# Kernel tuning notes

Measured on AMD Instinct MI355X. Metric: run time of the kernel, lower is better.

## Reference

```python
import jax, jax.numpy as jnp
import numpy as np
from jax import lax

EPS = 1e-5

def layer_norm(x, w, b):
    mu = x.mean(-1, keepdims=True)
    var = ((x - mu) ** 2).mean(-1, keepdims=True)
    return (x - mu) * lax.rsqrt(var + EPS) * w + b

def causal_dw_conv(x, w, b):
    # x: [B,L,D], w: [D,K] depthwise kernel, causal left pad
    B, L, D = x.shape
    K = w.shape[1]
    xt = jnp.pad(x.transpose(0, 2, 1), ((0, 0), (0, 0), (K - 1, 0)))  # [B,D,L+K-1]
    y = lax.conv_general_dilated(xt, w[:, None, :], (1,), 'VALID',
                                 dimension_numbers=('NCH', 'OIH', 'NCH'),
                                 feature_group_count=D)
    return (y + b[:, None]).transpose(0, 2, 1)

def mamba_block(x, ln_w, ln_b, W_in, b_in, conv_w, conv_b, W_xproj, W_dt, b_dt, A_log, Dp, W_out, b_out):
    res = x
    x = layer_norm(x, ln_w, ln_b)
    xz = x @ W_in + b_in                      # [B,L,2*Di]
    Di = xz.shape[-1] // 2
    xp, z = xz[..., :Di], xz[..., Di:]
    xp = jax.nn.silu(causal_dw_conv(xp, conv_w, conv_b))
    dbl = xp @ W_xproj                        # [B,L,R+2N]
    N = A_log.shape[-1]
    R = dbl.shape[-1] - 2 * N
    dt, Bm, Cm = dbl[..., :R], dbl[..., R:R + N], dbl[..., R + N:]
    delta = jax.nn.softplus(dt @ W_dt + b_dt)  # [B,L,Di]
    A = -jnp.exp(A_log)                        # [Di,N]
    dA = jnp.exp(delta[..., None] * A)                         # [B,L,Di,N]
    dBx = delta[..., None] * Bm[:, :, None, :] * xp[..., None]  # [B,L,Di,N]

    def step(h, inp):
        dAt, dBxt, ct = inp
        h = dAt * h + dBxt
        return h, jnp.einsum('bdn,bn->bd', h, ct)

    h0 = jnp.zeros((x.shape[0], Di, N), x.dtype)
    _, ys = lax.scan(step, h0, (dA.transpose(1, 0, 2, 3), dBx.transpose(1, 0, 2, 3), Cm.transpose(1, 0, 2)))
    y = ys.transpose(1, 0, 2) + xp * Dp        # [B,L,Di]
    y = y * jax.nn.silu(z)
    return res + y @ W_out + b_out

def reference(x, ln_w, ln_b, W_in, b_in, conv_w, conv_b, W_xproj, W_dt, b_dt, A_log, D, W_out, b_out, Wg, bg, Wv, bv):
    fwd = mamba_block(x, ln_w[0], ln_b[0], W_in[0], b_in[0], conv_w[0], conv_b[0], W_xproj[0], W_dt[0], b_dt[0], A_log[0], D[0], W_out[0], b_out[0])
    bwd = mamba_block(x[:, ::-1], ln_w[1], ln_b[1], W_in[1], b_in[1], conv_w[1], conv_b[1], W_xproj[1], W_dt[1], b_dt[1], A_log[1], D[1], W_out[1], b_out[1])
    bwd = bwd[:, ::-1]
    comb = jnp.concatenate([fwd, bwd], -1)
    gate = jax.nn.sigmoid(comb @ Wg + bg)
    value = comb @ Wv + bv
    return (gate * value + (1.0 - gate) * fwd + (1.0 - gate) * bwd) / 2.0

def setup_inputs() -> dict:
    B, L, Dm = 2, 1024, 1024
    Di, N, R, K = 2048, 16, 64, 4
    key = jax.random.key(0)
    ks = jax.random.split(key, 12)
    s_in = 1.0 / np.sqrt(Dm)
    s_di = 1.0 / np.sqrt(Di)
    A = jnp.broadcast_to(jnp.arange(1, N + 1, dtype=jnp.float32), (Di, N))
    return {
        'x': jax.random.normal(ks[0], (B, L, Dm), jnp.float32),
        'ln_w': jnp.ones((2, Dm), jnp.float32),
        'ln_b': jnp.zeros((2, Dm), jnp.float32),
        'W_in': jax.random.normal(ks[1], (2, Dm, 2 * Di), jnp.float32) * s_in,
        'b_in': jnp.zeros((2, 2 * Di), jnp.float32),
        'conv_w': jax.random.normal(ks[2], (2, Di, K), jnp.float32) * 0.5,
        'conv_b': jnp.zeros((2, Di), jnp.float32),
        'W_xproj': jax.random.normal(ks[3], (2, Di, R + 2 * N), jnp.float32) * s_di,
        'W_dt': jax.random.normal(ks[4], (2, R, Di), jnp.float32) * 0.02,
        'b_dt': jnp.full((2, Di), -4.6, jnp.float32) + 0.1 * jax.random.normal(ks[5], (2, Di), jnp.float32),
        'A_log': jnp.log(jnp.stack([A, A])),
        'D': jnp.ones((2, Di), jnp.float32),
        'W_out': jax.random.normal(ks[6], (2, Di, Dm), jnp.float32) * s_di,
        'b_out': jnp.zeros((2, Dm), jnp.float32),
        'Wg': jax.random.normal(ks[7], (2 * Dm, Dm), jnp.float32) / np.sqrt(2 * Dm),
        'bg': jnp.zeros((Dm,), jnp.float32),
        'Wv': jax.random.normal(ks[8], (2 * Dm, Dm), jnp.float32) / np.sqrt(2 * Dm),
        'bv': jnp.zeros((Dm,), jnp.float32),
    }
```

## Files before the change

### kernel.cpp

```cpp
#include <hip/hip_runtime.h>
#include <math.h>

constexpr int BB = 2;
constexpr int LL = 1024;
constexpr int DM = 1024;
constexpr int DI = 2048;
constexpr int NS = 16;
constexpr int RR = 64;
constexpr int MROWS = BB * LL;

constexpr int CLEN = 32;
constexpr int NCH = LL / CLEN;

constexpr int LDT = 40;
constexpr int NSPLIT = 16;
constexpr int KCH = DI / NSPLIT;

#define DEV __device__ __forceinline__

typedef unsigned short ushort_t;
using bf16x8 = __attribute__((ext_vector_type(8))) short;
using f32x4  = __attribute__((ext_vector_type(4))) float;

DEV float sigmoidf_(float x) { return 1.f / (1.f + expf(-x)); }
DEV float siluf_(float x) { return x * sigmoidf_(x); }
DEV float fast_softplus(float x) {
    return fmaxf(x, 0.f) + __logf(1.f + __expf(-fabsf(x)));
}

DEV ushort_t f2bf(float x) {
    union { float f; unsigned u; } v; v.f = x;
    unsigned r = v.u + 0x7FFFu + ((v.u >> 16) & 1u);
    return (ushort_t)(r >> 16);
}
DEV float bf2f(ushort_t u) {
    union { unsigned u; float f; } v; v.u = ((unsigned)u) << 16;
    return v.f;
}

typedef const __attribute__((address_space(1))) unsigned int* gptr_t;
typedef __attribute__((address_space(3))) unsigned int* lptr_t;
DEV void gload16(const void* g, void* l) {
    __builtin_amdgcn_global_load_lds((gptr_t)g, (lptr_t)l, 16, 0, 0);
}

template <int N> DEV void waitvm();
template <> DEV void waitvm<0>() { asm volatile("s_waitcnt vmcnt(0)" ::: "memory"); }
template <> DEV void waitvm<6>() { asm volatile("s_waitcnt vmcnt(6)" ::: "memory"); }
template <> DEV void waitvm<8>() { asm volatile("s_waitcnt vmcnt(8)" ::: "memory"); }
DEV void barrier_() { __builtin_amdgcn_s_barrier(); }

__global__ __launch_bounds__(256) void tcast(
    const float* __restrict__ in, long sIn,
    ushort_t* __restrict__ outT, long sOut,
    int R, int C)
{
    in += (size_t)blockIdx.z * sIn;
    outT += (size_t)blockIdx.z * sOut;
    __shared__ float tile[64][65];
    int r0 = blockIdx.y * 64, c0 = blockIdx.x * 64;
#pragma unroll
    for (int i = 0; i < 4; ++i) {
        int r = (threadIdx.x >> 4) + i * 16;
        int c4 = (threadIdx.x & 15) * 4;
        float4 v = *reinterpret_cast<const float4*>(&in[(size_t)(r0 + r) * C + c0 + c4]);
        tile[r][c4] = v.x; tile[r][c4 + 1] = v.y; tile[r][c4 + 2] = v.z; tile[r][c4 + 3] = v.w;
    }
    __syncthreads();
#pragma unroll
    for (int i = 0; i < 2; ++i) {
        int c = (threadIdx.x >> 3) + i * 32;
        int r8 = (threadIdx.x & 7) * 8;
        ushort_t o[8];
#pragma unroll
        for (int j = 0; j < 8; ++j) o[j] = f2bf(tile[r8 + j][c]);
        *reinterpret_cast<int4*>(&outT[(size_t)(c0 + c) * R + r0 + r8]) =
            *reinterpret_cast<int4*>(o);
    }
}

__global__ __launch_bounds__(256) void tcastP(
    const float* __restrict__ in, long sIn,
    ushort_t* __restrict__ outT, long sOut,
    int R, int C)
{
    in += (size_t)blockIdx.z * sIn;
    outT += (size_t)blockIdx.z * sOut;
    int idx = blockIdx.x * 256 + threadIdx.x;
    if (idx >= R * C) return;
    int r = idx / C, c = idx - r * C;
    outT[(size_t)c * R + r] = f2bf(in[idx]);
}

__global__ __launch_bounds__(256) void ln_kernel(
    const float* __restrict__ x,
    const float* __restrict__ ln_w,
    const float* __restrict__ ln_b,
    ushort_t* __restrict__ xlnb)
{
    int row = blockIdx.x;
    const float* xr = x + (size_t)row * DM;
    int i4 = threadIdx.x * 4;
    float4 v = *reinterpret_cast<const float4*>(&xr[i4]);
    float s = v.x + v.y + v.z + v.w;
    float s2 = v.x * v.x + v.y * v.y + v.z * v.z + v.w * v.w;
    for (int off = 32; off > 0; off >>= 1) {
        s += __shfl_down(s, off);
        s2 += __shfl_down(s2, off);
    }
    __shared__ float sbuf[10];
    int wid = threadIdx.x >> 6;
    if ((threadIdx.x & 63) == 0) { sbuf[wid] = s; sbuf[4 + wid] = s2; }
    __syncthreads();
    if (threadIdx.x == 0) {
        float S = sbuf[0] + sbuf[1] + sbuf[2] + sbuf[3];
        float S2 = sbuf[4] + sbuf[5] + sbuf[6] + sbuf[7];
        float mu = S / DM;
        float var = S2 / DM - mu * mu;
        sbuf[8] = mu;
        sbuf[9] = rsqrtf(var + 1e-5f);
    }
    __syncthreads();
    float mu = sbuf[8], rstd = sbuf[9];
    float nv0 = (v.x - mu) * rstd, nv1 = (v.y - mu) * rstd;
    float nv2 = (v.z - mu) * rstd, nv3 = (v.w - mu) * rstd;
#pragma unroll
    for (int d = 0; d < 2; ++d) {
        float4 w = *reinterpret_cast<const float4*>(&ln_w[d * DM + i4]);
        float4 b = *reinterpret_cast<const float4*>(&ln_b[d * DM + i4]);
        ushort_t o[4];
        o[0] = f2bf(nv0 * w.x + b.x);
        o[1] = f2bf(nv1 * w.y + b.y);
        o[2] = f2bf(nv2 * w.z + b.z);
        o[3] = f2bf(nv3 * w.w + b.w);
        *reinterpret_cast<uint2*>(&xlnb[(size_t)d * MROWS * DM + (size_t)row * DM + i4]) =
            *reinterpret_cast<uint2*>(o);
    }
}

__global__ __launch_bounds__(512, 1) void gemm_xpz256(
    const ushort_t* __restrict__ A,
    const ushort_t* __restrict__ Bt,
    const float* __restrict__ bias,
    ushort_t* __restrict__ xpb,
    ushort_t* __restrict__ zb)
{
    __shared__ ushort_t lds[4 * 256 * 64];

    int bid = blockIdx.x;
    int sid = (bid & 7) * 32 + (bid >> 3);
    int z = sid >> 7;
    int rem = sid & 127;
    int bx = rem >> 3;
    int by = rem & 7;
    int row0 = by * 256, col0 = bx * 256;

    A += (size_t)z * MROWS * DM;
    Bt += (size_t)z * (2 * DI) * DM;
    bias += (size_t)z * (2 * DI);
    xpb += (size_t)z * MROWS * DI;
    zb += (size_t)z * MROWS * DI;

    int tid = threadIdx.x;
    int lane = tid & 63;
    int w = tid >> 6;
    int wr = w >> 2, wc = w & 3;
    int lrow = lane & 15, lk = lane >> 4;
    int cr = lane >> 3, cs = lane & 7;

    f32x4 acc[8][4];
#pragma unroll
    for (int m = 0; m < 8; ++m)
#pragma unroll
        for (int n = 0; n < 4; ++n) acc[m][n] = {0.f, 0.f, 0.f, 0.f};

    auto stage = [&](int buf, int k0) {
        ushort_t* As_ = lds + buf * (256 * 64);
        ushort_t* Bs_ = lds + (2 + buf) * (256 * 64);
#pragma unroll
        for (int j = 0; j < 8; ++j) {
            int c = j * 8 + w;
            if (c < 32) {
                int r = c * 8 + cr;
                gload16(&A[(size_t)(row0 + r) * DM + k0 + ((cs ^ (r & 7)) * 8)],
                        As_ + c * 512);
            } else {
                int r = (c - 32) * 8 + cr;
                gload16(&Bt[(size_t)(col0 + r) * DM + k0 + ((cs ^ (r & 7)) * 8)],
                        Bs_ + (c - 32) * 512);
            }
        }
    };
    auto compute = [&](int buf) {
        const ushort_t* As_ = lds + buf * (256 * 64);
        const ushort_t* Bs_ = lds + (2 + buf) * (256 * 64);
#pragma unroll
        for (int kk = 0; kk < 2; ++kk) {
            int lkk = kk * 4 + lk;
            bf16x8 af[8], bfr[4];
#pragma unroll
            for (int m = 0; m < 8; ++m) {
                int ar = wr * 128 + m * 16 + lrow;
                af[m] = *reinterpret_cast<const bf16x8*>(&As_[ar * 64 + ((lkk ^ (ar & 7)) * 8)]);
            }
#pragma unroll
            for (int n = 0; n < 4; ++n) {
                int br = wc * 64 + n * 16 + lrow;
                bfr[n] = *reinterpret_cast<const bf16x8*>(&Bs_[br * 64 + ((lkk ^ (br & 7)) * 8)]);
            }
#pragma unroll
            for (int m = 0; m < 8; ++m)
#pragma unroll
                for (int n = 0; n < 4; ++n)
                    acc[m][n] = __builtin_amdgcn_mfma_f32_16x16x32_bf16(af[m], bfr[n], acc[m][n], 0, 0, 0);
        }
    };

    stage(0, 0);
    stage(1, 64);
    waitvm<8>();
    barrier_();
    for (int t = 0; t < 16; ++t) {
        int buf = t & 1;
        compute(buf);
        barrier_();
        int kn = (t + 2) * 64;
        if (kn < 1024) {
            stage(buf, kn);
            waitvm<8>();
        } else {
            waitvm<0>();
        }
        barrier_();
    }

    constexpr int EP2 = 264;
    ushort_t* dst = (col0 < DI) ? (xpb + col0) : (zb + (col0 - DI));
    __syncthreads();
#pragma unroll
    for (int h = 0; h < 2; ++h) {
        if (wr == h) {
#pragma unroll
            for (int n = 0; n < 4; ++n) {
                int col = wc * 64 + n * 16 + lrow;
                float bv = bias[col0 + col];
#pragma unroll
                for (int m = 0; m < 8; ++m)
#pragma unroll
                    for (int rr = 0; rr < 4; ++rr) {
                        int rl = m * 16 + lk * 4 + rr;
                        lds[rl * EP2 + col] = f2bf(acc[m][n][rr] + bv);
                    }
            }
        }
        __syncthreads();
#pragma unroll
        for (int q = 0; q < 8; ++q) {
            int lin = q * 512 + tid;
            int r = lin >> 5, c8 = lin & 31;
            *reinterpret_cast<int4*>(&dst[(size_t)(row0 + h * 128 + r) * DI + c8 * 8]) =
                *reinterpret_cast<int4*>(&lds[r * EP2 + c8 * 8]);
        }
        __syncthreads();
    }
}

enum { EPI_XPZ = 0, EPI_COMB = 1, EPI_SOFT = 2 };

template <int BM, int EPI>
__global__ __launch_bounds__(256) void gemm_as(
    const ushort_t* __restrict__ A, int lda, long sA,
    const ushort_t* __restrict__ Bt, int ldb, long sB,
    const float* __restrict__ bias, long sBias,
    ushort_t* __restrict__ outB, long sOutB,
    ushort_t* __restrict__ outB2, long sOutB2,
    const float* __restrict__ res,
    int ldout, int Kdim)
{
    constexpr int FM = BM / 32;
    constexpr int CA = BM / 8;
    constexpr int CT = CA + 16;
    constexpr int LW = CT / 4;
    __shared__ ushort_t lds[2 * BM * 64 + 2 * 128 * 64];

    int z = blockIdx.z;
    A += (size_t)z * sA; Bt += (size_t)z * sB; bias += (size_t)z * sBias;
    outB += (size_t)z * sOutB;
    if (outB2) outB2 += (size_t)z * sOutB2;

    int tid = threadIdx.x;
    int lane = tid & 63;
    int w = tid >> 6, wr = w >> 1, wc = w & 1;
    int lrow = lane & 15, lk = lane >> 4;
    int cr = lane >> 3, cs = lane & 7;
    int row0 = blockIdx.y * BM, col0 = blockIdx.x * 128;

    f32x4 acc[FM][4];
#pragma unroll
    for (int m = 0; m < FM; ++m)
#pragma unroll
        for (int n = 0; n < 4; ++n) acc[m][n] = {0.f, 0.f, 0.f, 0.f};

    auto stage = [&](int buf, int k0) {
        ushort_t* As_ = lds + buf * (BM * 64);
        ushort_t* Bs_ = lds + 2 * BM * 64 + buf * (128 * 64);
#pragma unroll
        for (int j = 0; j < CT / 4; ++j) {
            int c = j * 4 + w;
            if (c < CA) {
                int r = c * 8 + cr;
                gload16(&A[(size_t)(row0 + r) * lda + k0 + ((cs ^ (r & 7)) * 8)],
                        As_ + c * 512);
            } else {
                int r = (c - CA) * 8 + cr;
                gload16(&Bt[(size_t)(col0 + r) * ldb + k0 + ((cs ^ (r & 7)) * 8)],
                        Bs_ + (c - CA) * 512);
            }
        }
    };
    auto compute = [&](int buf) {
        const ushort_t* As_ = lds + buf * (BM * 64);
        const ushort_t* Bs_ = lds + 2 * BM * 64 + buf * (128 * 64);
#pragma unroll
        for (int kk = 0; kk < 2; ++kk) {
            int lkk = kk * 4 + lk;
            bf16x8 af[FM], bfr[4];
#pragma unroll
            for (int m = 0; m < FM; ++m) {
                int ar = wr * (BM / 2) + m * 16 + lrow;
                af[m] = *reinterpret_cast<const bf16x8*>(&As_[ar * 64 + ((lkk ^ (ar & 7)) * 8)]);
            }
#pragma unroll
            for (int n = 0; n < 4; ++n) {
                int br = wc * 64 + n * 16 + lrow;
                bfr[n] = *reinterpret_cast<const bf16x8*>(&Bs_[br * 64 + ((lkk ^ (br & 7)) * 8)]);
            }
#pragma unroll
            for (int m = 0; m < FM; ++m)
#pragma unroll
                for (int n = 0; n < 4; ++n)
                    acc[m][n] = __builtin_amdgcn_mfma_f32_16x16x32_bf16(af[m], bfr[n], acc[m][n], 0, 0, 0);
        }
    };

    stage(0, 0);
    if (Kdim > 64) {
        stage(1, 64);
        waitvm<LW>();
    } else {
        waitvm<0>();
    }
    barrier_();
    int nt = Kdim >> 6;
    for (int t = 0; t < nt; ++t) {
        int buf = t & 1;
        compute(buf);
        barrier_();
        int kn = (t + 2) * 64;
        if (kn < Kdim) {
            stage(buf, kn);
            waitvm<LW>();
        } else {
            waitvm<0>();
        }
        barrier_();
    }

    constexpr int EP = 136;
    __syncthreads();
#pragma unroll
    for (int n = 0; n < 4; ++n) {
        int col = wc * 64 + n * 16 + lrow;
        float bv = bias[col0 + col];
#pragma unroll
        for (int m = 0; m < FM; ++m) {
#pragma unroll
            for (int rr = 0; rr < 4; ++rr) {
                int rl = wr * (BM / 2) + m * 16 + lk * 4 + rr;
                float v = acc[m][n][rr] + bv;
                if constexpr (EPI == EPI_COMB)
                    v += res[(size_t)(row0 + rl) * DM + col0 + col];
                else if constexpr (EPI == EPI_SOFT)
                    v = fast_softplus(v);
                lds[rl * EP + col] = f2bf(v);
            }
        }
    }
    __syncthreads();
    const ushort_t* dst;
    if constexpr (EPI == EPI_XPZ) dst = (col0 < DI) ? outB + col0 : outB2 + (col0 - DI);
    else dst = outB + col0;
    constexpr int NI = BM * 16 / 256;
#pragma unroll
    for (int q = 0; q < NI; ++q) {
        int lin = q * 256 + tid;
        int r = lin >> 4, c8 = lin & 15;
        *reinterpret_cast<int4*>(const_cast<ushort_t*>(&dst[(size_t)(row0 + r) * ldout + c8 * 8])) =
            *reinterpret_cast<int4*>(&lds[r * EP + c8 * 8]);
    }
}

__global__ __launch_bounds__(256) void gemm_final64(
    const ushort_t* __restrict__ combb,
    const ushort_t* __restrict__ Bg,
    const ushort_t* __restrict__ Bv,
    const float* __restrict__ bgp, const float* __restrict__ bvp,
    float* __restrict__ out)
{
    __shared__ ushort_t lds[6 * 64 * 64];

    int tid = threadIdx.x;
    int lane = tid & 63;
    int w = tid >> 6, wr = w >> 1, wc = w & 1;
    int lrow = lane & 15, lk = lane >> 4;
    int cr = lane >> 3, cs = lane & 7;
    int row0 = blockIdx.y * 64, col0 = blockIdx.x * 64;

    f32x4 accg[2][2], accv[2][2];
#pragma unroll
    for (int m = 0; m < 2; ++m)
#pragma unroll
        for (int n = 0; n < 2; ++n) { accg[m][n] = {0.f,0.f,0.f,0.f}; accv[m][n] = {0.f,0.f,0.f,0.f}; }

    auto stage = [&](int buf, int k0) {
        ushort_t* As_  = lds + buf * 4096;
        ushort_t* Bs1_ = lds + 8192 + buf * 4096;
        ushort_t* Bs2_ = lds + 16384 + buf * 4096;
#pragma unroll
        for (int j = 0; j < 6; ++j) {
            int c = j * 4 + w;
            if (c < 8) {
                int r = c * 8 + cr;
                gload16(&combb[(size_t)(row0 + r) * (2 * DM) + k0 + ((cs ^ (r & 7)) * 8)],
                        As_ + c * 512);
            } else if (c < 16) {
                int r = (c - 8) * 8 + cr;
                gload16(&Bg[(size_t)(col0 + r) * (2 * DM) + k0 + ((cs ^ (r & 7)) * 8)],
                        Bs1_ + (c - 8) * 512);
            } else {
                int r = (c - 16) * 8 + cr;
                gload16(&Bv[(size_t)(col0 + r) * (2 * DM) + k0 + ((cs ^ (r & 7)) * 8)],
                        Bs2_ + (c - 16) * 512);
            }
        }
    };
    auto compute = [&](int buf) {
        const ushort_t* As_  = lds + buf * 4096;
        const ushort_t* Bs1_ = lds + 8192 + buf * 4096;
        const ushort_t* Bs2_ = lds + 16384 + buf * 4096;
#pragma unroll
        for (int kk = 0; kk < 2; ++kk) {
            int lkk = kk * 4 + lk;
            bf16x8 af[2], b1[2], b2[2];
#pragma unroll
            for (int m = 0; m < 2; ++m) {
                int ar = wr * 32 + m * 16 + lrow;
                af[m] = *reinterpret_cast<const bf16x8*>(&As_[ar * 64 + ((lkk ^ (ar & 7)) * 8)]);
            }
#pragma unroll
            for (int n = 0; n < 2; ++n) {
                int br = wc * 32 + n * 16 + lrow;
                b1[n] = *reinterpret_cast<const bf16x8*>(&Bs1_[br * 64 + ((lkk ^ (br & 7)) * 8)]);
                b2[n] = *reinterpret_cast<const bf16x8*>(&Bs2_[br * 64 + ((lkk ^ (br & 7)) * 8)]);
            }
#pragma unroll
            for (int m = 0; m < 2; ++m)
#pragma unroll
                for (int n = 0; n < 2; ++n) {
                    accg[m][n] = __builtin_amdgcn_mfma_f32_16x16x32_bf16(af[m], b1[n], accg[m][n], 0, 0, 0);
                    accv[m][n] = __builtin_amdgcn_mfma_f32_16x16x32_bf16(af[m], b2[n], accv[m][n], 0, 0, 0);
                }
        }
    };

    stage(0, 0);
    stage(1, 64);
    waitvm<6>();
    barrier_();
    for (int t = 0; t < 32; ++t) {
        int buf = t & 1;
        compute(buf);
        barrier_();
        int kn = (t + 2) * 64;
        if (kn < 2 * DM) {
            stage(buf, kn);
            waitvm<6>();
        } else {
            waitvm<0>();
        }
        barrier_();
    }

    constexpr int EPF = 68;
    float* epf = (float*)lds;
    __syncthreads();
#pragma unroll
    for (int n = 0; n < 2; ++n) {
        int col = wc * 32 + n * 16 + lrow;
        float bgv = bgp[col0 + col];
        float bvv = bvp[col0 + col];
#pragma unroll
        for (int m = 0; m < 2; ++m) {
#pragma unroll
            for (int rr = 0; rr < 4; ++rr) {
                int rl = wr * 32 + m * 16 + lk * 4 + rr;
                float g = sigmoidf_(accg[m][n][rr] + bgv);
                float v = accv[m][n][rr] + bvv;
                float f = bf2f(combb[(size_t)(row0 + rl) * (2 * DM) + col0 + col]);
                float wv2 = bf2f(combb[(size_t)(row0 + rl) * (2 * DM) + DM + col0 + col]);
                epf[rl * EPF + col] = 0.5f * (g * v + (1.f - g) * (f + wv2));
            }
        }
    }
    __syncthreads();
#pragma unroll
    for (int q = 0; q < 4; ++q) {
        int lin = q * 256 + tid;
        int r = lin >> 4, c4 = lin & 15;
        *reinterpret_cast<float4*>(&out[(size_t)(row0 + r) * DM + col0 + c4 * 4]) =
            *reinterpret_cast<float4*>(&epf[r * EPF + c4 * 4]);
    }
}

__global__ __launch_bounds__(256) void gemm_xproj(
    const ushort_t* __restrict__ A,
    const ushort_t* __restrict__ Bt,
    float* __restrict__ part)
{
    int z = blockIdx.z;
    A += (size_t)z * MROWS * DI;
    Bt += (size_t)z * 96 * DI;
    part += (size_t)z * NSPLIT * MROWS * 96;

    __shared__ ushort_t As[128 * LDT];
    __shared__ ushort_t Bs[96 * LDT];
    int tid = threadIdx.x;
    int lane = tid & 63;
    int w = tid >> 6, wr = w >> 1, wc = w & 1;
    int lrow = lane & 15, lk = lane >> 4;
    int s = blockIdx.x, rt = blockIdx.y;
    int row0 = rt * 128;
    int k0 = s * KCH;

    f32x4 acc[4][3];
#pragma unroll
    for (int m = 0; m < 4; ++m)
#pragma unroll
        for (int n = 0; n < 3; ++n) acc[m][n] = {0.f, 0.f, 0.f, 0.f};

    int sr = tid >> 2, ss = tid & 3;
    const ushort_t* ga0 = A + (size_t)(row0 + sr) * DI + k0 + ss * 8;
    const ushort_t* ga1 = A + (size_t)(row0 + sr + 64) * DI + k0 + ss * 8;

    for (int kk = 0; kk < KCH; kk += 32) {
        int4 a0 = *reinterpret_cast<const int4*>(ga0);
        int4 a1 = *reinterpret_cast<const int4*>(ga1);
        ga0 += 32; ga1 += 32;
        __syncthreads();
        *reinterpret_cast<int4*>(&As[sr * LDT + ss * 8]) = a0;
        *reinterpret_cast<int4*>(&As[(sr + 64) * LDT + ss * 8]) = a1;
        for (int i = tid; i < 96 * 4; i += 256) {
            int br = i >> 2, bs = i & 3;
            *reinterpret_cast<int4*>(&Bs[br * LDT + bs * 8]) =
                *reinterpret_cast<const int4*>(&Bt[(size_t)br * DI + k0 + kk + bs * 8]);
        }
        __syncthreads();
        bf16x8 af[4], bfr[3];
#pragma unroll
        for (int m = 0; m < 4; ++m)
            af[m] = *reinterpret_cast<const bf16x8*>(&As[(wr * 64 + m * 16 + lrow) * LDT + lk * 8]);
#pragma unroll
        for (int n = 0; n < 3; ++n)
            bfr[n] = *reinterpret_cast<const bf16x8*>(&Bs[(wc * 48 + n * 16 + lrow) * LDT + lk * 8]);
#pragma unroll
        for (int m = 0; m < 4; ++m)
#pragma unroll
            for (int n = 0; n < 3; ++n)
                acc[m][n] = __builtin_amdgcn_mfma_f32_16x16x32_bf16(af[m], bfr[n], acc[m][n], 0, 0, 0);
    }

#pragma unroll
    for (int n = 0; n < 3; ++n) {
        int col = wc * 48 + n * 16 + lrow;
#pragma unroll
        for (int m = 0; m < 4; ++m) {
#pragma unroll
            for (int rr = 0; rr < 4; ++rr) {
                int row = row0 + wr * 64 + m * 16 + lk * 4 + rr;
                part[((size_t)s * MROWS + row) * 96 + col] = acc[m][n][rr];
            }
        }
    }
}

__global__ __launch_bounds__(256) void dbl_reduce(
    const float* __restrict__ part,
    float* __restrict__ dblf,
    ushort_t* __restrict__ dtb)
{
    int idx = blockIdx.x * 256 + threadIdx.x;
    int d = idx / (MROWS * 96);
    int rem = idx - d * (MROWS * 96);
    int row = rem / 96, col = rem - row * 96;
    const float* p = part + (size_t)d * NSPLIT * MROWS * 96;
    float v = 0.f;
#pragma unroll
    for (int s = 0; s < NSPLIT; ++s)
        v += p[((size_t)s * MROWS + row) * 96 + col];
    dblf[idx] = v;
    if (col < RR) dtb[(size_t)d * MROWS * RR + (size_t)row * RR + col] = f2bf(v);
}

__global__ __launch_bounds__(256) void conv_silu_kernel(
    const ushort_t* __restrict__ xpb,
    const float* __restrict__ cw,
    const float* __restrict__ cb,
    ushort_t* __restrict__ xpcb)
{
    int d = blockIdx.y;
    xpb += (size_t)d * MROWS * DI;
    cw += (size_t)d * DI * 4;
    cb += (size_t)d * DI;
    xpcb += (size_t)d * MROWS * DI;
    int idx = blockIdx.x * 256 + threadIdx.x;
    int c = idx & (DI - 1);
    int row = idx >> 11;
    int t = row & (LL - 1);
    int b = row >> 10;
    float w0 = cw[c * 4 + 0], w1 = cw[c * 4 + 1], w2 = cw[c * 4 + 2], w3 = cw[c * 4 + 3];
    float acc = cb[c];
    if (!d) {
#pragma unroll
        for (int k = 0; k < 4; ++k) {
            int tt = t - 3 + k;
            if (tt >= 0) {
                float wv = (k == 0) ? w0 : (k == 1) ? w1 : (k == 2) ? w2 : w3;
                acc = fmaf(wv, bf2f(xpb[(size_t)(b * LL + tt) * DI + c]), acc);
            }
        }
    } else {
#pragma unroll
        for (int k = 0; k < 4; ++k) {
            int tt = t + 3 - k;
            if (tt < LL) {
                float wv = (k == 0) ? w0 : (k == 1) ? w1 : (k == 2) ? w2 : w3;
                acc = fmaf(wv, bf2f(xpb[(size_t)(b * LL + tt) * DI + c]), acc);
            }
        }
    }
    xpcb[idx] = f2bf(siluf_(acc));
}

__global__ __launch_bounds__(256) void scan_part1(
    const ushort_t* __restrict__ deltab,
    const ushort_t* __restrict__ xpcb,
    const float* __restrict__ dblf,
    const float* __restrict__ A_log,
    float* __restrict__ chunkS,
    ushort_t* __restrict__ chunkH)
{
    int zz = blockIdx.z;
    int d = zz >> 1, b = zz & 1;
    const ushort_t* delta_d = deltab + (size_t)d * MROWS * DI;
    const ushort_t* xpc_d = xpcb + (size_t)d * MROWS * DI;
    const float* dbl_d = dblf + (size_t)d * MROWS * 96;
    const float* Alg = A_log + (size_t)d * DI * NS;
    int reverse = d;

    int c = blockIdx.x * 256 + threadIdx.x;
    int ch = blockIdx.y;
    int base = b * LL;

    __shared__ float sB[CLEN][16];
    for (int r = threadIdx.x >> 4; r < CLEN; r += 16) {
        int col = threadIdx.x & 15;
        int i = ch * CLEN + r;
        int t = reverse ? (LL - 1 - i) : i;
        sB[r][col] = dbl_d[(size_t)(base + t) * 96 + RR + col];
    }
    __syncthreads();

    float Ac[NS];
#pragma unroll
    for (int q = 0; q < 4; ++q) {
        float4 a = *reinterpret_cast<const float4*>(&Alg[(size_t)c * NS + q * 4]);
        Ac[q * 4 + 0] = -__expf(a.x);
        Ac[q * 4 + 1] = -__expf(a.y);
        Ac[q * 4 + 2] = -__expf(a.z);
        Ac[q * 4 + 3] = -__expf(a.w);
    }
    float h[NS] = {};
    float S = 0.f;
    for (int ii = 0; ii < CLEN; ++ii) {
        int i = ch * CLEN + ii;
        int t = reverse ? (LL - 1 - i) : i;
        size_t row = (size_t)(base + t);
        float dlt = bf2f(delta_d[row * DI + c]);
        float xv = bf2f(xpc_d[row * DI + c]);
        S += dlt;
        float dx = dlt * xv;
        float4 B0 = *reinterpret_cast<const float4*>(&sB[ii][0]);
        float4 B1 = *reinterpret_cast<const float4*>(&sB[ii][4]);
        float4 B2 = *reinterpret_cast<const float4*>(&sB[ii][8]);
        float4 B3 = *reinterpret_cast<const float4*>(&sB[ii][12]);
        float Bv[NS] = {B0.x, B0.y, B0.z, B0.w, B1.x, B1.y, B1.z, B1.w,
                        B2.x, B2.y, B2.z, B2.w, B3.x, B3.y, B3.z, B3.w};
#pragma unroll
        for (int n = 0; n < NS; ++n)
            h[n] = fmaf(__expf(dlt * Ac[n]), h[n], dx * Bv[n]);
    }
    size_t sidx = ((size_t)((d * BB + b) * NCH + ch)) * DI + c;
    chunkS[sidx] = S;
    ushort_t o[16];
#pragma unroll
    for (int n = 0; n < NS; ++n) o[n] = f2bf(h[n]);
    ushort_t* hp = chunkH + sidx * NS;
    *reinterpret_cast<int4*>(&hp[0]) = *reinterpret_cast<int4*>(&o[0]);
    *reinterpret_cast<int4*>(&hp[8]) = *reinterpret_cast<int4*>(&o[8]);
}

__global__ __launch_bounds__(256) void scan_part2(
    ushort_t* __restrict__ chunkH,
    const float* __restrict__ chunkS,
    const float* __restrict__ A_log)
{
    int idx = blockIdx.x * 256 + threadIdx.x;
    int d = idx >> 16;
    int r = idx & 65535;
    int n = r & 15;
    int c = (r >> 4) & (DI - 1);
    int b = r >> 15;
    float Ac = -__expf(A_log[(size_t)d * DI * NS + (size_t)c * NS + n]);
    float cur = 0.f;
    for (int j = 0; j < NCH; ++j) {
        size_t sidx = ((size_t)((d * BB + b) * NCH + j)) * DI + c;
        float S = chunkS[sidx];
        float hf = bf2f(chunkH[sidx * NS + n]);
        float nxt = fmaf(__expf(Ac * S), cur, hf);
        chunkH[sidx * NS + n] = f2bf(cur);
        cur = nxt;
    }
}

__global__ __launch_bounds__(256) void scan_part3(
    const ushort_t* __restrict__ deltab,
    const ushort_t* __restrict__ xpcb,
    const float* __restrict__ dblf,
    const ushort_t* __restrict__ zbuf,
    const float* __restrict__ A_log,
    const float* __restrict__ Dp,
    const ushort_t* __restrict__ chunkH,
    ushort_t* __restrict__ ybufb)
{
    int zz = blockIdx.z;
    int d = zz >> 1, b = zz & 1;
    const ushort_t* delta_d = deltab + (size_t)d * MROWS * DI;
    const ushort_t* xpc_d = xpcb + (size_t)d * MROWS * DI;
    const float* dbl_d = dblf + (size_t)d * MROWS * 96;
    const ushort_t* z_d = zbuf + (size_t)d * MROWS * DI;
    const float* Alg = A_log + (size_t)d * DI * NS;
    const float* Dp_d = Dp + (size_t)d * DI;
    ushort_t* y_d = ybufb + (size_t)d * MROWS * DI;
    int reverse = d;

    int c = blockIdx.x * 256 + threadIdx.x;
    int ch = blockIdx.y;
    int base = b * LL;

    __shared__ float sBC[CLEN][32];
    for (int r = threadIdx.x >> 5; r < CLEN; r += 8) {
        int col = threadIdx.x & 31;
        int i = ch * CLEN + r;
        int t = reverse ? (LL - 1 - i) : i;
        sBC[r][col] = dbl_d[(size_t)(base + t) * 96 + RR + col];
    }
    __syncthreads();

    float Ac[NS];
#pragma unroll
    for (int q = 0; q < 4; ++q) {
        float4 a = *reinterpret_cast<const float4*>(&Alg[(size_t)c * NS + q * 4]);
        Ac[q * 4 + 0] = -__expf(a.x);
        Ac[q * 4 + 1] = -__expf(a.y);
        Ac[q * 4 + 2] = -__expf(a.z);
        Ac[q * 4 + 3] = -__expf(a.w);
    }
    size_t sidx = ((size_t)((d * BB + b) * NCH + ch)) * DI + c;
    const ushort_t* hp = chunkH + sidx * NS;
    int4 h0 = *reinterpret_cast<const int4*>(&hp[0]);
    int4 h1 = *reinterpret_cast<const int4*>(&hp[8]);
    const ushort_t* hs0 = reinterpret_cast<const ushort_t*>(&h0);
    const ushort_t* hs1 = reinterpret_cast<const ushort_t*>(&h1);
    float h[NS];
#pragma unroll
    for (int n = 0; n < 8; ++n) { h[n] = bf2f(hs0[n]); h[8 + n] = bf2f(hs1[n]); }
    float Dc = Dp_d[c];
    for (int ii = 0; ii < CLEN; ++ii) {
        int i = ch * CLEN + ii;
        int t = reverse ? (LL - 1 - i) : i;
        size_t row = (size_t)(base + t);
        float dlt = bf2f(delta_d[row * DI + c]);
        float xv = bf2f(xpc_d[row * DI + c]);
        float dx = dlt * xv;
        float4 B0 = *reinterpret_cast<const float4*>(&sBC[ii][0]);
        float4 B1 = *reinterpret_cast<const float4*>(&sBC[ii][4]);
        float4 B2 = *reinterpret_cast<const float4*>(&sBC[ii][8]);
        float4 B3 = *reinterpret_cast<const float4*>(&sBC[ii][12]);
        float4 C0 = *reinterpret_cast<const float4*>(&sBC[ii][16]);
        float4 C1 = *reinterpret_cast<const float4*>(&sBC[ii][20]);
        float4 C2 = *reinterpret_cast<const float4*>(&sBC[ii][24]);
        float4 C3 = *reinterpret_cast<const float4*>(&sBC[ii][28]);
        float Bv[NS] = {B0.x, B0.y, B0.z, B0.w, B1.x, B1.y, B1.z, B1.w,
                        B2.x, B2.y, B2.z, B2.w, B3.x, B3.y, B3.z, B3.w};
        float Cv[NS] = {C0.x, C0.y, C0.z, C0.w, C1.x, C1.y, C1.z, C1.w,
                        C2.x, C2.y, C2.z, C2.w, C3.x, C3.y, C3.z, C3.w};
        float y = 0.f;
#pragma unroll
        for (int n = 0; n < NS; ++n) {
            h[n] = fmaf(__expf(dlt * Ac[n]), h[n], dx * Bv[n]);
            y = fmaf(h[n], Cv[n], y);
        }
        float z = bf2f(z_d[row * DI + c]);
        y_d[row * DI + c] = f2bf((y + xv * Dc) * siluf_(z));
    }
}

extern "C" void kernel_launch(void* const* d_in, const int* in_sizes, int n_in,
                              void* d_out, int out_size, void* d_ws, size_t ws_size,
                              hipStream_t stream)
{
    const float* x      = (const float*)d_in[0];
    const float* ln_w   = (const float*)d_in[1];
    const float* ln_b   = (const float*)d_in[2];
    const float* W_in   = (const float*)d_in[3];
    const float* b_in   = (const float*)d_in[4];
    const float* conv_w = (const float*)d_in[5];
    const float* conv_b = (const float*)d_in[6];
    const float* W_xproj= (const float*)d_in[7];
    const float* W_dt   = (const float*)d_in[8];
    const float* b_dt   = (const float*)d_in[9];
    const float* A_log  = (const float*)d_in[10];
    const float* Dp     = (const float*)d_in[11];
    const float* W_out  = (const float*)d_in[12];
    const float* b_out  = (const float*)d_in[13];
    const float* Wg     = (const float*)d_in[14];
    const float* bg     = (const float*)d_in[15];
    const float* Wv     = (const float*)d_in[16];
    const float* bv     = (const float*)d_in[17];
    float* out = (float*)d_out;

    ushort_t* sb = (ushort_t*)d_ws;
    size_t o = 0;
    ushort_t* R0 = sb + o;
    ushort_t* xlnb = R0;
    ushort_t* xpb  = R0 + (size_t)2 * MROWS * DM;
    o += (size_t)2 * MROWS * DM + (size_t)2 * MROWS * DI;
    float* part = (float*)R0;
    ushort_t* ybufb = R0;
    ushort_t* zb     = sb + o; o += (size_t)2 * MROWS * DI;
    ushort_t* xpcb   = sb + o; o += (size_t)2 * MROWS * DI;
    ushort_t* deltab = sb + o; o += (size_t)2 * MROWS * DI;
    ushort_t* chHb   = sb + o; o += (size_t)2 * BB * NCH * DI * NS;
    ushort_t* combb  = sb + o; o += (size_t)MROWS * 2 * DM;
    float* dblf = (float*)combb;
    ushort_t* dtb = combb + (size_t)2 * (2 * MROWS * 96);
    float* chS = (float*)(combb + (size_t)2 * (2 * MROWS * 96) + (size_t)2 * MROWS * RR);
    ushort_t* WTin   = sb + o; o += (size_t)2 * (2 * DI) * DM;
    ushort_t* WTout  = sb + o; o += (size_t)2 * DM * DI;
    ushort_t* WTgv   = sb + o; o += (size_t)2 * DM * (2 * DM);
    ushort_t* WTxp   = sb + o; o += (size_t)2 * 96 * DI;
    ushort_t* WTdt   = sb + o; o += (size_t)2 * DI * RR;

    tcast<<<dim3(DM / 64, DI / 64, 2), 256, 0, stream>>>(
        W_out, (long)DI * DM, WTout, (long)DM * DI, DI, DM);
    tcast<<<dim3(DM / 64, (2 * DM) / 64, 1), 256, 0, stream>>>(
        Wg, 0, WTgv, 0, 2 * DM, DM);
    tcast<<<dim3(DM / 64, (2 * DM) / 64, 1), 256, 0, stream>>>(
        Wv, 0, WTgv + (size_t)DM * 2 * DM, 0, 2 * DM, DM);
    tcast<<<dim3(DI / 64, RR / 64, 2), 256, 0, stream>>>(
        W_dt, (long)RR * DI, WTdt, (long)DI * RR, RR, DI);
    tcastP<<<dim3((DI * 96 + 255) / 256, 1, 2), 256, 0, stream>>>(
        W_xproj, (long)DI * 96, WTxp, (long)96 * DI, DI, 96);
    tcast<<<dim3((2 * DI) / 64, DM / 64, 2), 256, 0, stream>>>(
        W_in, (long)DM * 2 * DI, WTin, (long)(2 * DI) * DM, DM, 2 * DI);

    ln_kernel<<<MROWS, 256, 0, stream>>>(x, ln_w, ln_b, xlnb);

    gemm_xpz256<<<256, 512, 0, stream>>>(xlnb, WTin, b_in, xpb, zb);

    conv_silu_kernel<<<dim3((MROWS * DI) / 256, 2), 256, 0, stream>>>(
        xpb, conv_w, conv_b, xpcb);

    gemm_xproj<<<dim3(NSPLIT, MROWS / 128, 2), 256, 0, stream>>>(xpcb, WTxp, part);
    dbl_reduce<<<(2 * MROWS * 96) / 256, 256, 0, stream>>>(part, dblf, dtb);

    gemm_as<128, EPI_SOFT><<<dim3(DI / 128, MROWS / 128, 2), 256, 0, stream>>>(
        dtb, RR, (long)MROWS * RR, WTdt, RR, (long)DI * RR,
        b_dt, DI, deltab, (long)MROWS * DI, nullptr, 0, nullptr, DI, RR);

    scan_part1<<<dim3(DI / 256, NCH, 4), 256, 0, stream>>>(
        deltab, xpcb, dblf, A_log, chS, chHb);
    scan_part2<<<(2 * BB * DI * NS) / 256, 256, 0, stream>>>(chHb, chS, A_log);
    scan_part3<<<dim3(DI / 256, NCH, 4), 256, 0, stream>>>(
        deltab, xpcb, dblf, zb, A_log, Dp, chHb, ybufb);

    gemm_as<64, EPI_COMB><<<dim3(DM / 128, MROWS / 64, 2), 256, 0, stream>>>(
        ybufb, DI, (long)MROWS * DI, WTout, DI, (long)DM * DI,
        b_out, DM, combb, DM, nullptr, 0, x, 2 * DM, DI);

    gemm_final64<<<dim3(DM / 64, MROWS / 64), 256, 0, stream>>>(
        combb, WTgv, WTgv + (size_t)DM * 2 * DM, bg, bv, out);
}
```

Measured before the change: 266.7 us.

## Interleave global-to-LDS staging with MFMA column phases in xpz GEMM main loop

Restructures the in_proj GEMM main loop so the next tiles' global_load_lds requests are split into A and B sub-stages and issued between the four per-column MFMA phases, rather than all at once after compute. It also loads all A fragments up front, waits on lgkmcnt, uses sched_barrier to pin the instruction order and raises wave priority around MFMA bursts. The goal is to overlap memory traffic with matrix math and smooth issue pressure. The cost is extra barriers per iteration (one per column phase) and tighter reasoning about buffer reuse and vmcnt accounting.

```diff
diff --git a/kernel.cpp b/kernel.cpp
--- a/kernel.cpp
+++ b/kernel.cpp
@@ -48,7 +48,9 @@
 template <> DEV void waitvm<0>() { asm volatile("s_waitcnt vmcnt(0)" ::: "memory"); }
 template <> DEV void waitvm<6>() { asm volatile("s_waitcnt vmcnt(6)" ::: "memory"); }
 template <> DEV void waitvm<8>() { asm volatile("s_waitcnt vmcnt(8)" ::: "memory"); }
+DEV void lgkm0() { asm volatile("s_waitcnt lgkmcnt(0)" ::: "memory"); }
 DEV void barrier_() { __builtin_amdgcn_s_barrier(); }
+DEV void sched0() { __builtin_amdgcn_sched_barrier(0); }
 
 __global__ __launch_bounds__(256) void tcast(
     const float* __restrict__ in, long sIn,
@@ -146,6 +148,7 @@
     ushort_t* __restrict__ zb)
 {
     __shared__ ushort_t lds[4 * 256 * 64];
+    constexpr int NT = 16;
 
     int bid = blockIdx.x;
     int sid = (bid & 7) * 32 + (bid >> 3);
@@ -174,64 +177,89 @@
 #pragma unroll
         for (int n = 0; n < 4; ++n) acc[m][n] = {0.f, 0.f, 0.f, 0.f};
 
-    auto stage = [&](int buf, int k0) {
-        ushort_t* As_ = lds + buf * (256 * 64);
-        ushort_t* Bs_ = lds + (2 + buf) * (256 * 64);
-#pragma unroll
-        for (int j = 0; j < 8; ++j) {
-            int c = j * 8 + w;
-            if (c < 32) {
-                int r = c * 8 + cr;
-                gload16(&A[(size_t)(row0 + r) * DM + k0 + ((cs ^ (r & 7)) * 8)],
-                        As_ + c * 512);
-            } else {
-                int r = (c - 32) * 8 + cr;
-                gload16(&Bt[(size_t)(col0 + r) * DM + k0 + ((cs ^ (r & 7)) * 8)],
-                        Bs_ + (c - 32) * 512);
-            }
-        }
+    auto gA = [&](int s, int k0, int c) {
+        int r = c * 8 + cr;
+        gload16(&A[(size_t)(row0 + r) * DM + k0 + ((cs ^ (r & 7)) * 8)],
+                lds + s * (256 * 64) + c * 512);
     };
-    auto compute = [&](int buf) {
-        const ushort_t* As_ = lds + buf * (256 * 64);
-        const ushort_t* Bs_ = lds + (2 + buf) * (256 * 64);
-#pragma unroll
-        for (int kk = 0; kk < 2; ++kk) {
-            int lkk = kk * 4 + lk;
-            bf16x8 af[8], bfr[4];
-#pragma unroll
-            for (int m = 0; m < 8; ++m) {
-                int ar = wr * 128 + m * 16 + lrow;
-                af[m] = *reinterpret_cast<const bf16x8*>(&As_[ar * 64 + ((lkk ^ (ar & 7)) * 8)]);
-            }
-#pragma unroll
-            for (int n = 0; n < 4; ++n) {
-                int br = wc * 64 + n * 16 + lrow;
-                bfr[n] = *reinterpret_cast<const bf16x8*>(&Bs_[br * 64 + ((lkk ^ (br & 7)) * 8)]);
-            }
+    auto gB = [&](int s, int k0, int c) {
+        int r = c * 8 + cr;
+        gload16(&Bt[(size_t)(col0 + r) * DM + k0 + ((cs ^ (r & 7)) * 8)],
+                lds + (2 + s) * (256 * 64) + c * 512);
+    };
+    auto stage_A = [&](int t) {
+        int s = t & 1, k0 = t * 64;
+#pragma unroll
+        for (int j = 0; j < 4; ++j) gA(s, k0, w * 4 + j);
+    };
+    auto stage_Bn01 = [&](int t) {
+        int s = t & 1, k0 = t * 64;
+#pragma unroll
+        for (int j = 0; j < 2; ++j) {
+            int idx = w * 2 + j;
+            gB(s, k0, (idx >> 2) * 8 + (idx & 3));
+        }
+    };
+    auto stage_Bn2 = [&](int t) {
+        int s = t & 1, k0 = t * 64;
+        gB(s, k0, (w >> 1) * 8 + 4 + (w & 1));
+    };
+    auto stage_Bn3 = [&](int t) {
+        int s = t & 1, k0 = t * 64;
+        gB(s, k0, (w >> 1) * 8 + 6 + (w & 1));
+    };
+
+    stage_A(0); stage_Bn01(0); stage_Bn2(0); stage_Bn3(0);
+    stage_A(1); stage_Bn01(1); stage_Bn2(1);
+
+    for (int t = 0; t < NT; ++t) {
+        int s = t & 1;
+        const ushort_t* As_ = lds + s * (256 * 64);
+        const ushort_t* Bs_ = lds + (2 + s) * (256 * 64);
+
+        barrier_();
+        sched0();
+        if (t + 1 < NT) stage_Bn3(t + 1);
+        if (t == NT - 1) waitvm<0>(); else waitvm<8>();
+        barrier_();
+        sched0();
+
+        bf16x8 af[8][2];
+#pragma unroll
+        for (int n = 0; n < 4; ++n) {
+            if (n == 1 && t + 2 < NT) stage_A(t + 2);
+            if (n == 2 && t + 2 < NT) stage_Bn01(t + 2);
+            if (n == 3 && t + 2 < NT) stage_Bn2(t + 2);
+            if (n == 0) {
+#pragma unroll
+                for (int m = 0; m < 8; ++m) {
+                    int ar = wr * 128 + m * 16 + lrow;
+#pragma unroll
+                    for (int kk = 0; kk < 2; ++kk) {
+                        int lkk = kk * 4 + lk;
+                        af[m][kk] = *reinterpret_cast<const bf16x8*>(
+                            &As_[ar * 64 + ((lkk ^ (ar & 7)) * 8)]);
+                    }
+                }
+            }
+            int br = wc * 64 + n * 16 + lrow;
+            bf16x8 b0 = *reinterpret_cast<const bf16x8*>(
+                &Bs_[br * 64 + (((0 * 4 + lk) ^ (br & 7)) * 8)]);
+            bf16x8 b1 = *reinterpret_cast<const bf16x8*>(
+                &Bs_[br * 64 + (((1 * 4 + lk) ^ (br & 7)) * 8)]);
+            lgkm0();
+            sched0();
+            __builtin_amdgcn_s_setprio(1);
 #pragma unroll
             for (int m = 0; m < 8; ++m)
-#pragma unroll
-                for (int n = 0; n < 4; ++n)
-                    acc[m][n] = __builtin_amdgcn_mfma_f32_16x16x32_bf16(af[m], bfr[n], acc[m][n], 0, 0, 0);
-        }
-    };
-
-    stage(0, 0);
-    stage(1, 64);
-    waitvm<8>();
-    barrier_();
-    for (int t = 0; t < 16; ++t) {
-        int buf = t & 1;
-        compute(buf);
-        barrier_();
-        int kn = (t + 2) * 64;
-        if (kn < 1024) {
-            stage(buf, kn);
-            waitvm<8>();
-        } else {
-            waitvm<0>();
-        }
-        barrier_();
+                acc[m][n] = __builtin_amdgcn_mfma_f32_16x16x32_bf16(af[m][0], b0, acc[m][n], 0, 0, 0);
+#pragma unroll
+            for (int m = 0; m < 8; ++m)
+                acc[m][n] = __builtin_amdgcn_mfma_f32_16x16x32_bf16(af[m][1], b1, acc[m][n], 0, 0, 0);
+            __builtin_amdgcn_s_setprio(0);
+            barrier_();
+            sched0();
+        }
     }
 
     constexpr int EP2 = 264;
```

New measurement: 265.5 us. About the same (-0.5%).
